# Kernel tuning notes

Hardware: AMD Instinct MI355X
Metric: run time of the kernel (lower is better)

Reference implementation:

```python
import jax, jax.numpy as jnp
import numpy as np

NUM_EXPERTS = 16
TOP_K = 2
AUX_LOSS_COEF = 0.01


def setup_inputs() -> dict:
    key = jax.random.key(0)
    ks = jax.random.split(key, 5)
    B, S, D, I, E = 4, 2048, 1024, 2816, NUM_EXPERTS
    scale = 0.02
    return {
        "x": jax.random.normal(ks[0], (B, S, D), dtype=jnp.float32),
        "gate_w": jax.random.normal(ks[1], (D, E), dtype=jnp.float32) * scale,
        "Wg": jax.random.normal(ks[2], (E, D, I), dtype=jnp.float32) * scale,
        "Wu": jax.random.normal(ks[3], (E, D, I), dtype=jnp.float32) * scale,
        "Wd": jax.random.normal(ks[4], (E, I, D), dtype=jnp.float32) * scale,
    }


def _moe_forward(x, gate_w, Wg, Wu, Wd):
    B, S, D = x.shape
    E = gate_w.shape[1]
    # Router
    logits = x @ gate_w                      # [B,S,E]
    probs = jax.nn.softmax(logits, axis=-1)  # [B,S,E]
    topk_w, topk_idx = jax.lax.top_k(probs, TOP_K)        # [B,S,K]
    topk_w = topk_w / jnp.sum(topk_w, axis=-1, keepdims=True)
    # Per-token combine weight for each expert: [B,S,E]
    onehot = jax.nn.one_hot(topk_idx, E, dtype=x.dtype)   # [B,S,K,E]
    combine_w = jnp.einsum("bsk,bske->bse", topk_w, onehot)
    x_flat = x.reshape(-1, D)                # [T,D]
    w_flat = combine_w.reshape(-1, E)        # [T,E]
    # Accumulate weighted expert outputs (loop over fixed small E; unselected
    # tokens get zero weight, identical math to masked gather/scatter).
    out = jnp.zeros_like(x_flat)
    for e in range(E):
        h = jax.nn.silu(x_flat @ Wg[e]) * (x_flat @ Wu[e])  # [T,I]
        out = out + (h @ Wd[e]) * w_flat[:, e:e + 1]
    out = out.reshape(B, S, D)
    # Load balancing aux loss
    expert_mask = onehot.sum(axis=2)                        # [B,S,E]
    tokens_per_expert = expert_mask.mean(axis=(0, 1))       # [E]
    router_prob_per_expert = probs.mean(axis=(0, 1))        # [E]
    aux_loss = AUX_LOSS_COEF * jnp.sum(tokens_per_expert * router_prob_per_expert) * E
    return out, aux_loss


def reference(x, gate_w, Wg, Wu, Wd):
    return _moe_forward(x, gate_w, Wg, Wu, Wd)
```

## Files before the change

### kernel.cpp

```cpp
#include <hip/hip_runtime.h>
#include <stdint.h>

#define T_TOKENS 8192
#define D_DIM 1024
#define I_DIM 2816
#define E_NUM 16
#define N_SLOTS 16384

typedef float f32x4 __attribute__((ext_vector_type(4)));
typedef short s16x8 __attribute__((ext_vector_type(8)));
typedef short s16x4 __attribute__((ext_vector_type(4)));
typedef unsigned short u16;
typedef unsigned int u32;

__device__ __forceinline__ u16 f2bf(float f) {
  u32 u = __builtin_bit_cast(u32, f);
  u = (u + 0x7FFFu + ((u >> 16) & 1u)) >> 16;
  return (u16)u;
}
__device__ __forceinline__ u32 pack2(float a, float b) {
  return (u32)f2bf(a) | ((u32)f2bf(b) << 16);
}
__device__ __forceinline__ void async_load16(const void* g, void* l) {
  __builtin_amdgcn_global_load_lds(
      (const __attribute__((address_space(1))) void*)g,
      (__attribute__((address_space(3))) void*)l, 16, 0, 0);
}

__global__ void router_kernel(const float* __restrict__ x,
                              const float* __restrict__ gw,
                              int* __restrict__ e12, float* __restrict__ w12,
                              int* __restrict__ cnt, float* __restrict__ probsum) {
  __shared__ float sProb[E_NUM];
  __shared__ int sCnt[E_NUM];
  int tid = threadIdx.x;
  if (tid < E_NUM) { sProb[tid] = 0.f; sCnt[tid] = 0; }
  __syncthreads();
  int g = tid >> 4, i = tid & 15;
  int t = blockIdx.x * 16 + g;
  float acc[E_NUM];
#pragma unroll
  for (int e = 0; e < E_NUM; e++) acc[e] = 0.f;
  const f32x4* x4 = (const f32x4*)(x + (size_t)t * D_DIM);
  const f32x4* g4 = (const f32x4*)gw;
  for (int jj = 0; jj < 16; jj++) {
    f32x4 xv = x4[i + 16 * jj];
    int jb = 4 * (i + 16 * jj);
#pragma unroll
    for (int r = 0; r < 4; r++) {
      float xs = xv[r];
#pragma unroll
      for (int e4 = 0; e4 < 4; e4++) {
        f32x4 gv = g4[(jb + r) * 4 + e4];
        acc[e4 * 4 + 0] += xs * gv[0];
        acc[e4 * 4 + 1] += xs * gv[1];
        acc[e4 * 4 + 2] += xs * gv[2];
        acc[e4 * 4 + 3] += xs * gv[3];
      }
    }
  }
#pragma unroll
  for (int e = 0; e < E_NUM; e++) {
    float v = acc[e];
    v += __shfl_down(v, 8, 16);
    v += __shfl_down(v, 4, 16);
    v += __shfl_down(v, 2, 16);
    v += __shfl_down(v, 1, 16);
    acc[e] = v;
  }
  if (i == 0) {
    float mx = acc[0];
#pragma unroll
    for (int e = 1; e < E_NUM; e++) mx = fmaxf(mx, acc[e]);
    float p[E_NUM]; float s = 0.f;
#pragma unroll
    for (int e = 0; e < E_NUM; e++) { p[e] = __expf(acc[e] - mx); s += p[e]; }
    float inv = 1.f / s;
#pragma unroll
    for (int e = 0; e < E_NUM; e++) p[e] *= inv;
    int e1 = 0; float p1 = p[0];
#pragma unroll
    for (int e = 1; e < E_NUM; e++) if (p[e] > p1) { p1 = p[e]; e1 = e; }
    int e2 = (e1 == 0) ? 1 : 0; float p2 = p[e2];
#pragma unroll
    for (int e = 0; e < E_NUM; e++) if (e != e1 && p[e] > p2) { p2 = p[e]; e2 = e; }
    float wsum = p1 + p2;
    e12[2 * t] = e1; e12[2 * t + 1] = e2;
    w12[2 * t] = p1 / wsum; w12[2 * t + 1] = p2 / wsum;
#pragma unroll
    for (int e = 0; e < E_NUM; e++) atomicAdd(&sProb[e], p[e]);
    atomicAdd(&sCnt[e1], 1);
    atomicAdd(&sCnt[e2], 1);
  }
  __syncthreads();
  if (tid < E_NUM) {
    atomicAdd(&cnt[tid], sCnt[tid]);
    atomicAdd(&probsum[tid], sProb[tid]);
  }
}

__global__ void prefix_kernel(const int* __restrict__ cnt, int* __restrict__ offsets,
                              const float* __restrict__ probsum, float* __restrict__ aux_out) {
  if (threadIdx.x == 0) {
    int s = 0;
    for (int e = 0; e < E_NUM; e++) { offsets[e] = s; s += cnt[e]; }
    offsets[E_NUM] = s;
    float a = 0.f;
    for (int e = 0; e < E_NUM; e++) a += (float)cnt[e] * probsum[e];
    aux_out[0] = 0.01f * 16.f * a / (8192.f * 8192.f);
  }
}

__global__ void build_kernel(const int* __restrict__ e12, const float* __restrict__ w12,
                             const int* __restrict__ offsets, int* __restrict__ cursor,
                             int* __restrict__ tlist, float* __restrict__ wlist,
                             int* __restrict__ slot2) {
  int t = blockIdx.x * 256 + threadIdx.x;
  if (t >= T_TOKENS) return;
#pragma unroll
  for (int k = 0; k < 2; k++) {
    int e = e12[2 * t + k];
    int pos = atomicAdd(&cursor[e], 1);
    int idx = offsets[e] + pos;
    tlist[idx] = t;
    wlist[idx] = w12[2 * t + k];
    slot2[2 * t + k] = idx;
  }
}

__global__ void gather_kernel(const float* __restrict__ x, const int* __restrict__ tlist,
                              u16* __restrict__ Xe) {
  int r = blockIdx.x * 4 + (threadIdx.x >> 6);
  int lane = threadIdx.x & 63;
  int tok = tlist[r];
  const f32x4* src = (const f32x4*)(x + (size_t)tok * D_DIM);
  u32* dst = (u32*)(Xe + (size_t)r * D_DIM);
#pragma unroll
  for (int c = 0; c < 4; c++) {
    f32x4 v = src[lane + 64 * c];
    dst[(lane + 64 * c) * 2] = pack2(v[0], v[1]);
    dst[(lane + 64 * c) * 2 + 1] = pack2(v[2], v[3]);
  }
}

template <int K, int N>
__global__ __launch_bounds__(256) void transpose_kernel(const float* __restrict__ W,
                                                        u16* __restrict__ Wt) {
  __shared__ u16 tile[64][66];
  int e = blockIdx.z;
  int k0 = blockIdx.x * 64;
  int n0 = blockIdx.y * 64;
  const float* Win = W + (size_t)e * K * N;
  u16* Wout = Wt + (size_t)e * N * K;
  int t = threadIdx.x;
  int r = t >> 4;
  int c4 = (t & 15) * 4;
#pragma unroll
  for (int rep = 0; rep < 4; rep++) {
    int k = r + rep * 16;
    f32x4 v = *(const f32x4*)(Win + (size_t)(k0 + k) * N + n0 + c4);
    *(u32*)&tile[k][c4] = pack2(v[0], v[1]);
    *(u32*)&tile[k][c4 + 2] = pack2(v[2], v[3]);
  }
  __syncthreads();
#pragma unroll
  for (int rep = 0; rep < 4; rep++) {
    int n = r + rep * 16;
    int k4 = c4;
    s16x4 o;
    o[0] = tile[k4 + 0][n];
    o[1] = tile[k4 + 1][n];
    o[2] = tile[k4 + 2][n];
    o[3] = tile[k4 + 3][n];
    *(s16x4*)(Wout + (size_t)(n0 + n) * K + k0 + k4) = o;
  }
}

__global__ __launch_bounds__(512, 2) void gemm_gu_kernel(
    const u16* __restrict__ Abuf, const u16* __restrict__ Bg, const u16* __restrict__ Bu,
    u16* __restrict__ Hbuf,
    const int* __restrict__ cnt, const int* __restrict__ offsets) {
  int e = blockIdx.z;
  int Me = cnt[e];
  int m0 = blockIdx.y * 256;
  if (m0 >= Me) return;
  int n0 = blockIdx.x * 128;
  int rowBase = offsets[e];
  const u16* Bge = Bg + (size_t)e * I_DIM * D_DIM;
  const u16* Bue = Bu + (size_t)e * I_DIM * D_DIM;

  __shared__ u16 lds[65536];
  constexpr int A0 = 0, A1 = 16384;
  constexpr int Bg0 = 32768, Bg1 = 40960;
  constexpr int Bu0 = 49152, Bu1 = 57344;

  int tid = threadIdx.x;
  int lane = tid & 63;
  int wv = tid >> 6;
  int wm = wv >> 1;
  int wn = wv & 1;
  int lrow = lane & 15, lq = lane >> 4;
  int swz = lrow & 7;

  f32x4 accg[4][4], accu[4][4];
#pragma unroll
  for (int a = 0; a < 4; a++)
#pragma unroll
    for (int b = 0; b < 4; b++) { accg[a][b] = (f32x4)0.f; accu[a][b] = (f32x4)0.f; }

  auto STAGE = [&](int kt, int b) {
    int k0 = kt << 6;
#pragma unroll
    for (int r = 0; r < 4; r++) {
      int c = tid + 512 * r;
      int row = c >> 3, slot = c & 7;
      int gr = m0 + row; gr = (gr < Me) ? gr : (Me - 1);
      const u16* src = Abuf + (size_t)(rowBase + gr) * D_DIM + k0 + ((slot ^ (row & 7)) << 3);
      async_load16(src, (void*)&lds[(b ? A1 : A0) + (wv * 64 + 512 * r) * 8]);
    }
#pragma unroll
    for (int r = 0; r < 2; r++) {
      int c = tid + 512 * r;
      int row = c >> 3, slot = c & 7;
      int col = k0 + ((slot ^ (row & 7)) << 3);
      int ldso = (wv * 64 + 512 * r) * 8;
      async_load16(Bge + (size_t)(n0 + row) * D_DIM + col, (void*)&lds[(b ? Bg1 : Bg0) + ldso]);
      async_load16(Bue + (size_t)(n0 + row) * D_DIM + col, (void*)&lds[(b ? Bu1 : Bu0) + ldso]);
    }
  };

  STAGE(0, 0);
  STAGE(1, 1);

  for (int kt = 0; kt < 16; kt++) {
    int cur = kt & 1;
    if (kt < 15) asm volatile("s_waitcnt vmcnt(8)");
    else         asm volatile("s_waitcnt vmcnt(0)");
    __builtin_amdgcn_s_barrier();
    __builtin_amdgcn_sched_barrier(0);

    const u16* As = lds + (cur ? A1 : A0);
    const u16* Bgs = lds + (cur ? Bg1 : Bg0);
    const u16* Bus = lds + (cur ? Bu1 : Bu0);

#pragma unroll
    for (int kh = 0; kh < 2; kh++) {
      s16x8 af[4], bb[4];
      int so = ((kh * 4 + lq) ^ swz) << 3;
#pragma unroll
      for (int fm = 0; fm < 4; fm++) {
        int row = wm * 64 + fm * 16 + lrow;
        af[fm] = *(const s16x8*)&As[row * 64 + so];
      }
#pragma unroll
      for (int fn = 0; fn < 4; fn++) {
        int row = wn * 64 + fn * 16 + lrow;
        bb[fn] = *(const s16x8*)&Bgs[row * 64 + so];
      }
      __builtin_amdgcn_s_barrier();
      __builtin_amdgcn_s_setprio(1);
#pragma unroll
      for (int fm = 0; fm < 4; fm++)
#pragma unroll
        for (int fn = 0; fn < 4; fn++)
          accg[fm][fn] = __builtin_amdgcn_mfma_f32_16x16x32_bf16(af[fm], bb[fn], accg[fm][fn], 0, 0, 0);
      __builtin_amdgcn_s_setprio(0);
      __builtin_amdgcn_s_barrier();
#pragma unroll
      for (int fn = 0; fn < 4; fn++) {
        int row = wn * 64 + fn * 16 + lrow;
        bb[fn] = *(const s16x8*)&Bus[row * 64 + so];
      }
      __builtin_amdgcn_s_barrier();
      __builtin_amdgcn_s_setprio(1);
#pragma unroll
      for (int fm = 0; fm < 4; fm++)
#pragma unroll
        for (int fn = 0; fn < 4; fn++)
          accu[fm][fn] = __builtin_amdgcn_mfma_f32_16x16x32_bf16(af[fm], bb[fn], accu[fm][fn], 0, 0, 0);
      __builtin_amdgcn_s_setprio(0);
      __builtin_amdgcn_s_barrier();
    }

    __builtin_amdgcn_sched_barrier(0);
    if (kt + 2 < 16) STAGE(kt + 2, cur);
  }

#pragma unroll
  for (int fm = 0; fm < 4; fm++) {
#pragma unroll
    for (int i = 0; i < 4; i++) {
      int m = m0 + wm * 64 + fm * 16 + lq * 4 + i;
      if (m >= Me) continue;
      size_t arow = (size_t)(rowBase + m);
#pragma unroll
      for (int fn = 0; fn < 4; fn++) {
        int col = n0 + wn * 64 + fn * 16 + lrow;
        float g = accg[fm][fn][i];
        float u = accu[fm][fn][i];
        float h = (g / (1.f + __expf(-g))) * u;
        Hbuf[arow * I_DIM + col] = f2bf(h);
      }
    }
  }
}

__global__ __launch_bounds__(256) void gemm_down_kernel(
    const u16* __restrict__ Abuf, const u16* __restrict__ Bd, float* __restrict__ Y,
    const int* __restrict__ cnt, const int* __restrict__ offsets,
    const float* __restrict__ wlist) {
  int e = blockIdx.z;
  int Me = cnt[e];
  int m0 = blockIdx.y * 128;
  if (m0 >= Me) return;
  int n0 = blockIdx.x * 128;
  int rowBase = offsets[e];
  const u16* Bde = Bd + (size_t)e * D_DIM * I_DIM;

  __shared__ u16 Ash[128 * 32];
  __shared__ u16 Bsh[128 * 32];

  int tid = threadIdx.x;
  int lane = tid & 63;
  int wv = tid >> 6;
  int mq = wv & 1, nq = wv >> 1;
  int lrow = lane & 15, lq = lane >> 4;

  f32x4 acc[4][4];
#pragma unroll
  for (int a = 0; a < 4; a++)
#pragma unroll
    for (int b = 0; b < 4; b++) acc[a][b] = (f32x4)0.f;

  for (int k0 = 0; k0 < I_DIM; k0 += 32) {
#pragma unroll
    for (int rep = 0; rep < 2; rep++) {
      int idx = tid + 256 * rep;
      int row = idx >> 2, q = idx & 3;
      int ldso = (wv * 64 + 256 * rep) * 8;
      int gr = m0 + row;
      gr = (gr < Me) ? gr : (Me - 1);
      async_load16(Abuf + (size_t)(rowBase + gr) * I_DIM + k0 + q * 8, &Ash[ldso]);
      async_load16(Bde + (size_t)(n0 + row) * I_DIM + k0 + q * 8, &Bsh[ldso]);
    }
    __syncthreads();
    s16x8 af[4], bfr[4];
#pragma unroll
    for (int fm = 0; fm < 4; fm++)
      af[fm] = *(const s16x8*)&Ash[(mq * 64 + fm * 16 + lrow) * 32 + lq * 8];
#pragma unroll
    for (int fn = 0; fn < 4; fn++)
      bfr[fn] = *(const s16x8*)&Bsh[(nq * 64 + fn * 16 + lrow) * 32 + lq * 8];
#pragma unroll
    for (int fm = 0; fm < 4; fm++)
#pragma unroll
      for (int fn = 0; fn < 4; fn++)
        acc[fm][fn] = __builtin_amdgcn_mfma_f32_16x16x32_bf16(af[fm], bfr[fn], acc[fm][fn], 0, 0, 0);
    __syncthreads();
  }
#pragma unroll
  for (int fm = 0; fm < 4; fm++) {
#pragma unroll
    for (int i = 0; i < 4; i++) {
      int m = m0 + mq * 64 + fm * 16 + lq * 4 + i;
      if (m >= Me) continue;
      size_t arow = (size_t)(rowBase + m);
      float w = wlist[arow];
#pragma unroll
      for (int fn = 0; fn < 4; fn++) {
        int col = n0 + nq * 64 + fn * 16 + lrow;
        Y[arow * D_DIM + col] = acc[fm][fn][i] * w;
      }
    }
  }
}

__global__ __launch_bounds__(256) void combine_kernel(
    const float* __restrict__ Y, const int* __restrict__ slot2,
    float* __restrict__ out) {
  int t = blockIdx.x;
  int tid = threadIdx.x;
  int s1 = slot2[2 * t];
  int s2 = slot2[2 * t + 1];
  const f32x4* y1 = (const f32x4*)(Y + (size_t)s1 * D_DIM);
  const f32x4* y2 = (const f32x4*)(Y + (size_t)s2 * D_DIM);
  f32x4* o = (f32x4*)(out + (size_t)t * D_DIM);
  o[tid] = y1[tid] + y2[tid];
}

extern "C" void kernel_launch(void* const* d_in, const int* in_sizes, int n_in,
                              void* d_out, int out_size, void* d_ws, size_t ws_size,
                              hipStream_t stream) {
  const float* x  = (const float*)d_in[0];
  const float* gw = (const float*)d_in[1];
  const float* Wg = (const float*)d_in[2];
  const float* Wu = (const float*)d_in[3];
  const float* Wd = (const float*)d_in[4];
  float* outf = (float*)d_out;
  char* ws = (char*)d_ws;
  int*   cnt     = (int*)(ws + 0);
  int*   cursor  = (int*)(ws + 64);
  float* probsum = (float*)(ws + 128);
  int*   offsets = (int*)(ws + 192);
  int*   e12     = (int*)(ws + 512);
  float* w12     = (float*)(ws + 66048);
  int*   tlist   = (int*)(ws + 131584);
  float* wlist   = (float*)(ws + 197120);
  int*   slot2   = (int*)(ws + 262656);
  u16*   Xe      = (u16*)(ws + (1 << 20));
  u16*   H       = (u16*)(ws + 34603008);
  u16*   WtA     = (u16*)(ws + 134217728);
  u16*   WtB     = (u16*)(ws + 234881024);
  float* Y       = (float*)(ws + 234881024);

  hipMemsetAsync(d_ws, 0, 512, stream);

  router_kernel<<<512, 256, 0, stream>>>(x, gw, e12, w12, cnt, probsum);
  prefix_kernel<<<1, 64, 0, stream>>>(cnt, offsets, probsum, outf + (size_t)(T_TOKENS * D_DIM));
  build_kernel<<<32, 256, 0, stream>>>(e12, w12, offsets, cursor, tlist, wlist, slot2);
  gather_kernel<<<4096, 256, 0, stream>>>(x, tlist, Xe);

  transpose_kernel<D_DIM, I_DIM><<<dim3(16, 44, E_NUM), 256, 0, stream>>>(Wg, WtA);
  transpose_kernel<D_DIM, I_DIM><<<dim3(16, 44, E_NUM), 256, 0, stream>>>(Wu, WtB);

  gemm_gu_kernel<<<dim3(22, 32, E_NUM), 512, 0, stream>>>(Xe, WtA, WtB, H, cnt, offsets);

  transpose_kernel<I_DIM, D_DIM><<<dim3(44, 16, E_NUM), 256, 0, stream>>>(Wd, WtA);

  gemm_down_kernel<<<dim3(8, 64, E_NUM), 256, 0, stream>>>(H, WtA, Y, cnt, offsets, wlist);

  combine_kernel<<<T_TOKENS, 256, 0, stream>>>(Y, slot2, outf);
}
```

Before: 1.127 ms.

## Double-buffer and swizzle down-projection GEMM with larger tiles; widen transpose tiles

The down-projection GEMM now uses 512 threads with 256x128 tiles, a K step of 64, and two LDS buffers filled by async loads. An XOR swizzle avoids LDS bank conflicts, and explicit waitcnt, barriers and setprio let the prefetch of the next stage overlap the MFMA work. This is meant to hide global-load latency and cut barrier stalls compared with the old single-buffered 32-wide K loop. The weight transpose kernel now handles 64x256 tiles and writes 16-byte vectors, cutting the block count and making stores wider, at the cost of more LDS per block and possible bank conflicts on the column reads.

```diff
diff --git a/kernel.cpp b/kernel.cpp
--- a/kernel.cpp
+++ b/kernel.cpp
@@ -146,10 +146,10 @@
 template <int K, int N>
 __global__ __launch_bounds__(256) void transpose_kernel(const float* __restrict__ W,
                                                         u16* __restrict__ Wt) {
-  __shared__ u16 tile[64][66];
+  __shared__ u16 tile[64][258];
   int e = blockIdx.z;
   int k0 = blockIdx.x * 64;
-  int n0 = blockIdx.y * 64;
+  int n0 = blockIdx.y * 256;
   const float* Win = W + (size_t)e * K * N;
   u16* Wout = Wt + (size_t)e * N * K;
   int t = threadIdx.x;
@@ -158,21 +158,24 @@
 #pragma unroll
   for (int rep = 0; rep < 4; rep++) {
     int k = r + rep * 16;
-    f32x4 v = *(const f32x4*)(Win + (size_t)(k0 + k) * N + n0 + c4);
-    *(u32*)&tile[k][c4] = pack2(v[0], v[1]);
-    *(u32*)&tile[k][c4 + 2] = pack2(v[2], v[3]);
+    const float* rowp = Win + (size_t)(k0 + k) * N + n0;
+#pragma unroll
+    for (int s = 0; s < 4; s++) {
+      f32x4 v = *(const f32x4*)(rowp + s * 64 + c4);
+      *(u32*)&tile[k][s * 64 + c4] = pack2(v[0], v[1]);
+      *(u32*)&tile[k][s * 64 + c4 + 2] = pack2(v[2], v[3]);
+    }
   }
   __syncthreads();
 #pragma unroll
-  for (int rep = 0; rep < 4; rep++) {
-    int n = r + rep * 16;
-    int k4 = c4;
-    s16x4 o;
-    o[0] = tile[k4 + 0][n];
-    o[1] = tile[k4 + 1][n];
-    o[2] = tile[k4 + 2][n];
-    o[3] = tile[k4 + 3][n];
-    *(s16x4*)(Wout + (size_t)(n0 + n) * K + k0 + k4) = o;
+  for (int rep = 0; rep < 8; rep++) {
+    int c = t + 256 * rep;
+    int n = c >> 3;
+    int k8 = (c & 7) * 8;
+    s16x8 o;
+#pragma unroll
+    for (int i = 0; i < 8; i++) o[i] = tile[k8 + i][n];
+    *(s16x8*)(Wout + (size_t)(n0 + n) * K + k0 + k8) = o;
   }
 }
 
@@ -305,26 +308,29 @@
   }
 }
 
-__global__ __launch_bounds__(256) void gemm_down_kernel(
+__global__ __launch_bounds__(512, 2) void gemm_down_kernel(
     const u16* __restrict__ Abuf, const u16* __restrict__ Bd, float* __restrict__ Y,
     const int* __restrict__ cnt, const int* __restrict__ offsets,
     const float* __restrict__ wlist) {
   int e = blockIdx.z;
   int Me = cnt[e];
-  int m0 = blockIdx.y * 128;
+  int m0 = blockIdx.y * 256;
   if (m0 >= Me) return;
   int n0 = blockIdx.x * 128;
   int rowBase = offsets[e];
   const u16* Bde = Bd + (size_t)e * D_DIM * I_DIM;
 
-  __shared__ u16 Ash[128 * 32];
-  __shared__ u16 Bsh[128 * 32];
+  __shared__ u16 lds[49152];
+  constexpr int A0 = 0, A1 = 16384;
+  constexpr int B0 = 32768, B1 = 40960;
 
   int tid = threadIdx.x;
   int lane = tid & 63;
   int wv = tid >> 6;
-  int mq = wv & 1, nq = wv >> 1;
+  int wm = wv >> 1;
+  int wn = wv & 1;
   int lrow = lane & 15, lq = lane >> 4;
+  int swz = lrow & 7;
 
   f32x4 acc[4][4];
 #pragma unroll
@@ -332,43 +338,82 @@
 #pragma unroll
     for (int b = 0; b < 4; b++) acc[a][b] = (f32x4)0.f;
 
-  for (int k0 = 0; k0 < I_DIM; k0 += 32) {
-#pragma unroll
-    for (int rep = 0; rep < 2; rep++) {
-      int idx = tid + 256 * rep;
-      int row = idx >> 2, q = idx & 3;
-      int ldso = (wv * 64 + 256 * rep) * 8;
-      int gr = m0 + row;
-      gr = (gr < Me) ? gr : (Me - 1);
-      async_load16(Abuf + (size_t)(rowBase + gr) * I_DIM + k0 + q * 8, &Ash[ldso]);
-      async_load16(Bde + (size_t)(n0 + row) * I_DIM + k0 + q * 8, &Bsh[ldso]);
-    }
-    __syncthreads();
-    s16x8 af[4], bfr[4];
-#pragma unroll
-    for (int fm = 0; fm < 4; fm++)
-      af[fm] = *(const s16x8*)&Ash[(mq * 64 + fm * 16 + lrow) * 32 + lq * 8];
-#pragma unroll
-    for (int fn = 0; fn < 4; fn++)
-      bfr[fn] = *(const s16x8*)&Bsh[(nq * 64 + fn * 16 + lrow) * 32 + lq * 8];
-#pragma unroll
-    for (int fm = 0; fm < 4; fm++)
-#pragma unroll
-      for (int fn = 0; fn < 4; fn++)
-        acc[fm][fn] = __builtin_amdgcn_mfma_f32_16x16x32_bf16(af[fm], bfr[fn], acc[fm][fn], 0, 0, 0);
-    __syncthreads();
-  }
+  auto STAGE = [&](int kt, int b) {
+    int k0 = kt << 6;
+#pragma unroll
+    for (int r = 0; r < 4; r++) {
+      int c = tid + 512 * r;
+      int row = c >> 3, slot = c & 7;
+      int gr = m0 + row; gr = (gr < Me) ? gr : (Me - 1);
+      const u16* src = Abuf + (size_t)(rowBase + gr) * I_DIM + k0 + ((slot ^ (row & 7)) << 3);
+      async_load16(src, (void*)&lds[(b ? A1 : A0) + (wv * 64 + 512 * r) * 8]);
+    }
+    {
+      int r = 0;
+#pragma unroll
+      for (r = 0; r < 2; r++) {
+        int c = tid + 512 * r;
+        int row = c >> 3, slot = c & 7;
+        int col = k0 + ((slot ^ (row & 7)) << 3);
+        async_load16(Bde + (size_t)(n0 + row) * I_DIM + col,
+                     (void*)&lds[(b ? B1 : B0) + (wv * 64 + 512 * r) * 8]);
+      }
+    }
+  };
+
+  STAGE(0, 0);
+  STAGE(1, 1);
+
+  for (int kt = 0; kt < 44; kt++) {
+    int cur = kt & 1;
+    if (kt < 43) asm volatile("s_waitcnt vmcnt(6)");
+    else         asm volatile("s_waitcnt vmcnt(0)");
+    __builtin_amdgcn_s_barrier();
+    __builtin_amdgcn_sched_barrier(0);
+
+    const u16* As = lds + (cur ? A1 : A0);
+    const u16* Bs = lds + (cur ? B1 : B0);
+
+#pragma unroll
+    for (int kh = 0; kh < 2; kh++) {
+      s16x8 af[4], bb[4];
+      int so = ((kh * 4 + lq) ^ swz) << 3;
+#pragma unroll
+      for (int fm = 0; fm < 4; fm++) {
+        int row = wm * 64 + fm * 16 + lrow;
+        af[fm] = *(const s16x8*)&As[row * 64 + so];
+      }
+#pragma unroll
+      for (int fn = 0; fn < 4; fn++) {
+        int row = wn * 64 + fn * 16 + lrow;
+        bb[fn] = *(const s16x8*)&Bs[row * 64 + so];
+      }
+      __builtin_amdgcn_s_barrier();
+      __builtin_amdgcn_s_setprio(1);
+#pragma unroll
+      for (int fm = 0; fm < 4; fm++)
+#pragma unroll
+        for (int fn = 0; fn < 4; fn++)
+          acc[fm][fn] = __builtin_amdgcn_mfma_f32_16x16x32_bf16(af[fm], bb[fn], acc[fm][fn], 0, 0, 0);
+      __builtin_amdgcn_s_setprio(0);
+      __builtin_amdgcn_s_barrier();
+    }
+
+    __builtin_amdgcn_sched_barrier(0);
+    if (kt + 2 < 44) STAGE(kt + 2, cur);
+  }
+
 #pragma unroll
   for (int fm = 0; fm < 4; fm++) {
 #pragma unroll
     for (int i = 0; i < 4; i++) {
-      int m = m0 + mq * 64 + fm * 16 + lq * 4 + i;
+      int m = m0 + wm * 64 + fm * 16 + lq * 4 + i;
       if (m >= Me) continue;
       size_t arow = (size_t)(rowBase + m);
       float w = wlist[arow];
 #pragma unroll
       for (int fn = 0; fn < 4; fn++) {
-        int col = n0 + nq * 64 + fn * 16 + lrow;
+        int col = n0 + wn * 64 + fn * 16 + lrow;
         Y[arow * D_DIM + col] = acc[fm][fn][i] * w;
       }
     }
@@ -420,14 +465,14 @@
   build_kernel<<<32, 256, 0, stream>>>(e12, w12, offsets, cursor, tlist, wlist, slot2);
   gather_kernel<<<4096, 256, 0, stream>>>(x, tlist, Xe);
 
-  transpose_kernel<D_DIM, I_DIM><<<dim3(16, 44, E_NUM), 256, 0, stream>>>(Wg, WtA);
-  transpose_kernel<D_DIM, I_DIM><<<dim3(16, 44, E_NUM), 256, 0, stream>>>(Wu, WtB);
+  transpose_kernel<D_DIM, I_DIM><<<dim3(16, 11, E_NUM), 256, 0, stream>>>(Wg, WtA);
+  transpose_kernel<D_DIM, I_DIM><<<dim3(16, 11, E_NUM), 256, 0, stream>>>(Wu, WtB);
 
   gemm_gu_kernel<<<dim3(22, 32, E_NUM), 512, 0, stream>>>(Xe, WtA, WtB, H, cnt, offsets);
 
-  transpose_kernel<I_DIM, D_DIM><<<dim3(44, 16, E_NUM), 256, 0, stream>>>(Wd, WtA);
-
-  gemm_down_kernel<<<dim3(8, 64, E_NUM), 256, 0, stream>>>(H, WtA, Y, cnt, offsets, wlist);
+  transpose_kernel<I_DIM, D_DIM><<<dim3(44, 4, E_NUM), 256, 0, stream>>>(Wd, WtA);
+
+  gemm_down_kernel<<<dim3(8, 32, E_NUM), 512, 0, stream>>>(H, WtA, Y, cnt, offsets, wlist);
 
   combine_kernel<<<T_TOKENS, 256, 0, stream>>>(Y, slot2, outf);
 }
```

Result: no change. 1.134 ms (+0.7%).
